# Optimization experiments

Measured on AMD Instinct MI355X. Metric: run time of the kernel, lower is better.

Reference implementation:

```python
import jax, jax.numpy as jnp
import numpy as np

B, N, H, D, HS, RS = 4, 512, 16, 64, 1024, 64  # HS = H*D, HSIZE_INSIDE == HSIZE
SCALE = 1.0 / float(np.sqrt(D))


def setup_inputs() -> dict:
    key = jax.random.key(0)
    ks = jax.random.split(key, 11)
    s = 0.02
    return {
        "v": jax.random.normal(ks[0], (B, N, HS), jnp.float32),
        "k": jax.random.normal(ks[1], (B, N, HS), jnp.float32),
        "q": jax.random.normal(ks[2], (B, N, HS), jnp.float32),
        "mask": jax.random.randint(ks[3], (B, 1, N, N), 0, 2).astype(bool),
        "rel_embed": jax.random.uniform(ks[4], (B, N, N, RS), jnp.float32),
        # weights stored as [in, out] (torch Linear applies x @ W.T)
        "Wv": jax.random.normal(ks[5], (HS, HS), jnp.float32) * s,
        "Wk": jax.random.normal(ks[6], (HS, HS), jnp.float32) * s,
        "Wq": jax.random.normal(ks[7], (HS, HS), jnp.float32) * s,
        "Wr": jax.random.normal(ks[8], (RS, H), jnp.float32) * s,
        "br": jax.random.normal(ks[9], (H,), jnp.float32) * s,
        "Wm": jax.random.normal(ks[10], (HS, HS), jnp.float32) * s,
    }


def reference(v, k, q, mask, rel_embed, Wv, Wk, Wq, Wr, br, Wm):
    b, nq, _ = q.shape

    def proj(x, W):  # [b, n, HS] -> [b, H, n, D]
        return (x @ W).reshape(b, -1, H, D).transpose(0, 2, 1, 3)

    vh, kh, qh = proj(v, Wv), proj(k, Wk), proj(q, Wq)
    # learned relative-position bias: relu -> clamp -> log, [b, H, nq, nk]
    r = jax.nn.relu(rel_embed @ Wr + br)
    bias = jnp.log(jnp.clip(r, 1e-6, None)).transpose(0, 3, 1, 2)
    scores = jnp.einsum('bhqd,bhkd->bhqk', qh, kh) * SCALE + bias
    scores = jnp.where(mask, jnp.float32(-1e9), scores)
    att = jax.nn.softmax(scores, axis=-1)  # dropout_r = 0
    atted = jnp.einsum('bhqk,bhkd->bhqd', att, vh)
    atted = atted.transpose(0, 2, 1, 3).reshape(b, nq, H * D)
    return atted @ Wm
```

## Files before the change

### kernel.cpp

```cpp
#include <hip/hip_runtime.h>
#include <hip/hip_bf16.h>


typedef __bf16 bf16_t;
typedef __bf16 bf16x8 __attribute__((ext_vector_type(8)));
typedef float f32x4 __attribute__((ext_vector_type(4)));

__device__ __forceinline__ f32x4 mfma16(bf16x8 a, bf16x8 b, f32x4 c) {
  return __builtin_amdgcn_mfma_f32_16x16x32_bf16(a, b, c, 0, 0, 0);
}
__device__ __forceinline__ f32x4 zero4() {
  f32x4 z; z[0] = 0.f; z[1] = 0.f; z[2] = 0.f; z[3] = 0.f; return z;
}

#define GLOAD_LDS16(gptr, lptr)                                                   \
  __builtin_amdgcn_global_load_lds(                                               \
      (const __attribute__((address_space(1))) unsigned int*)(gptr),              \
      (__attribute__((address_space(3))) unsigned int*)(lptr), 16, 0, 0)

__global__ __launch_bounds__(256) void prep_kernel(
    const float* __restrict__ W0, const float* __restrict__ W1,
    const float* __restrict__ W2, const float* __restrict__ W3,
    bf16_t* __restrict__ OutBase,
    const float* __restrict__ q, const float* __restrict__ k, const float* __restrict__ v,
    bf16_t* __restrict__ Qc, bf16_t* __restrict__ Kc, bf16_t* __restrict__ Vc,
    const unsigned int* __restrict__ mw, int* __restrict__ flag) {
  const int tid = threadIdx.x;
  if (blockIdx.x >= 1024) {
    const size_t gid = (size_t)(blockIdx.x - 1024) * 256 + tid;
    const int which = (int)(gid >> 18);
    const size_t off = (gid & 262143) * 8;
    const float* src = which == 0 ? q : which == 1 ? k : v;
    bf16_t* dst = which == 0 ? Qc : which == 1 ? Kc : Vc;
    const float scl = which == 0 ? 0.125f : 1.0f;
    float4 f0 = *(const float4*)(src + off);
    float4 f1 = *(const float4*)(src + off + 4);
    bf16x8 o;
    o[0] = (bf16_t)(f0.x * scl); o[1] = (bf16_t)(f0.y * scl);
    o[2] = (bf16_t)(f0.z * scl); o[3] = (bf16_t)(f0.w * scl);
    o[4] = (bf16_t)(f1.x * scl); o[5] = (bf16_t)(f1.y * scl);
    o[6] = (bf16_t)(f1.z * scl); o[7] = (bf16_t)(f1.w * scl);
    *(bf16x8*)(dst + off) = o;
    return;
  }
  const int wz = blockIdx.x >> 8, wy = (blockIdx.x >> 4) & 15, wx = blockIdx.x & 15;
  const float* W = wz == 0 ? W0 : wz == 1 ? W1 : wz == 2 ? W2 : W3;
  bf16_t* Ot = OutBase + (size_t)wz * 1024 * 1024;
  __shared__ float tile[64][68];
  __shared__ int sflag;
  const bool probe = (blockIdx.x == 0);
  if (probe && tid == 0) sflag = 0;
  const int i0 = wy * 64, j0 = wx * 64;
  const int ri = tid >> 2, rc = (tid & 3) * 16;
  const float* src = W + (size_t)(i0 + ri) * 1024 + j0 + rc;
#pragma unroll
  for (int qq = 0; qq < 4; ++qq) {
    float4 f = *(const float4*)(src + qq * 4);
    *(float4*)(&tile[ri][rc + qq * 4]) = f;
  }
  if (probe) {
    int any = 0;
    for (int i = tid; i < 4096; i += 256) any |= (mw[i] > 1u) ? 1 : 0;
    if (any) atomicOr(&sflag, 1);
  }
  __syncthreads();
  const int wj = tid >> 2, wc = (tid & 3) * 16;
  bf16x8 o0, o1;
#pragma unroll
  for (int s = 0; s < 8; ++s) o0[s] = (bf16_t)tile[wc + s][wj];
#pragma unroll
  for (int s = 0; s < 8; ++s) o1[s] = (bf16_t)tile[wc + 8 + s][wj];
  bf16_t* dst = Ot + (size_t)(j0 + wj) * 1024 + i0 + wc;
  *(bf16x8*)dst = o0;
  *(bf16x8*)(dst + 8) = o1;
  if (probe && tid == 0) *flag = sflag;
}

__global__ __launch_bounds__(256) void fat_kernel(
    const float* __restrict__ rel, const float* __restrict__ Wr,
    const float* __restrict__ br, const void* __restrict__ mask,
    const int* __restrict__ mflag, bf16_t* __restrict__ biasM,
    const bf16_t* __restrict__ Aq, const bf16_t* __restrict__ Ak, const bf16_t* __restrict__ Av,
    const bf16_t* __restrict__ Bq, const bf16_t* __restrict__ Bk, const bf16_t* __restrict__ Bv,
    bf16_t* __restrict__ Oq, bf16_t* __restrict__ Ok, bf16_t* __restrict__ Ov) {
  __shared__ __align__(16) bf16_t Asm[128 * 64];
  __shared__ __align__(16) bf16_t Bsm[128 * 64];
  const int tid = threadIdx.x, wid = tid >> 6, lane = tid & 63;
  const int lg = lane >> 4, lc = lane & 15;

  if (blockIdx.x < 2048) {
    const int pair = blockIdx.x;
    const int b = pair >> 9, qrow = pair & 511;
    const int isU8 = *mflag;
    bf16x8 wf[2];
#pragma unroll
    for (int kk = 0; kk < 2; ++kk)
#pragma unroll
      for (int j = 0; j < 8; ++j)
        wf[kk][j] = (bf16_t)Wr[(kk * 32 + lg * 8 + j) * 16 + lc];
    float brv[4];
#pragma unroll
    for (int j = 0; j < 4; ++j) brv[j] = br[lg * 4 + j];
    const float* relrow = rel + (size_t)pair * 512 * 64;
    const size_t mbase = (size_t)b * 512 * 512 + (size_t)qrow * 512;
    bf16_t* outb = biasM + (size_t)b * 16 * 512 * 512 + (size_t)qrow * 512;
#pragma unroll 4
    for (int kt = wid * 8; kt < wid * 8 + 8; ++kt) {
      const int k0 = kt * 16;
      const float* rrow = relrow + (size_t)(k0 + lc) * 64;
      f32x4 acc;
      acc[0] = brv[0]; acc[1] = brv[1]; acc[2] = brv[2]; acc[3] = brv[3];
#pragma unroll
      for (int kk = 0; kk < 2; ++kk) {
        const float4* s = (const float4*)(rrow + kk * 32 + lg * 8);
        float4 f0 = s[0], f1 = s[1];
        bf16x8 bfr;
        bfr[0] = (bf16_t)f0.x; bfr[1] = (bf16_t)f0.y; bfr[2] = (bf16_t)f0.z; bfr[3] = (bf16_t)f0.w;
        bfr[4] = (bf16_t)f1.x; bfr[5] = (bf16_t)f1.y; bfr[6] = (bf16_t)f1.z; bfr[7] = (bf16_t)f1.w;
        acc = mfma16(wf[kk], bfr, acc);
      }
      bool mb;
      if (isU8) mb = ((const unsigned char*)mask)[mbase + k0 + lc] != 0;
      else      mb = ((const int*)mask)[mbase + k0 + lc] != 0;
#pragma unroll
      for (int j = 0; j < 4; ++j) {
        const float valf = mb ? -1e9f : __logf(fmaxf(acc[j], 1e-6f));
        outb[(size_t)(lg * 4 + j) * 512 * 512 + k0 + lc] = (bf16_t)valf;
      }
    }
    return;
  }

  const int idx = blockIdx.x - 2048;
  const int z = idx >> 7, rem = idx & 127;
  const int byy = rem >> 3, bxx = rem & 7;
  const bf16_t* A = (z == 0) ? Aq : (z == 1) ? Ak : Av;
  const bf16_t* Bt = (z == 0) ? Bq : (z == 1) ? Bk : Bv;
  bf16_t* Out = (z == 0) ? Oq : (z == 1) ? Ok : Ov;
  const int m0 = byy * 128, n0 = bxx * 128;
  const int wm = (wid >> 1) * 64, wn = (wid & 1) * 64;
  const int sr = lane >> 3;
  const int scch = lane & 7;
  const int srcch = scch ^ sr;
  const bf16_t* Ap[4];
  const bf16_t* Bp[4];
#pragma unroll
  for (int i = 0; i < 4; ++i) {
    const int r = wid * 32 + i * 8 + sr;
    Ap[i] = A + (size_t)(m0 + r) * 1024 + srcch * 8;
    Bp[i] = Bt + (size_t)(n0 + r) * 1024 + srcch * 8;
  }
  f32x4 acc[4][4];
#pragma unroll
  for (int i = 0; i < 4; ++i)
#pragma unroll
    for (int j = 0; j < 4; ++j) acc[i][j] = zero4();

  for (int k0 = 0; k0 < 1024; k0 += 64) {
#pragma unroll
    for (int i = 0; i < 4; ++i) {
      GLOAD_LDS16(Ap[i] + k0, Asm + (wid * 32 + i * 8) * 64);
      GLOAD_LDS16(Bp[i] + k0, Bsm + (wid * 32 + i * 8) * 64);
    }
    __syncthreads();
#pragma unroll
    for (int kk = 0; kk < 2; ++kk) {
      bf16x8 af[4], bfv[4];
#pragma unroll
      for (int i = 0; i < 4; ++i) {
        const int ar = wm + i * 16 + lc;
        af[i] = *(const bf16x8*)(Asm + ar * 64 + ((kk * 4 + lg) ^ (ar & 7)) * 8);
        const int brr = wn + i * 16 + lc;
        bfv[i] = *(const bf16x8*)(Bsm + brr * 64 + ((kk * 4 + lg) ^ (brr & 7)) * 8);
      }
#pragma unroll
      for (int mi = 0; mi < 4; ++mi)
#pragma unroll
        for (int ni = 0; ni < 4; ++ni) acc[mi][ni] = mfma16(af[mi], bfv[ni], acc[mi][ni]);
    }
    __syncthreads();
  }
#pragma unroll
  for (int mi = 0; mi < 4; ++mi)
#pragma unroll
    for (int ni = 0; ni < 4; ++ni)
#pragma unroll
      for (int j = 0; j < 4; ++j) {
        const int m = m0 + wm + mi * 16 + lg * 4 + j;
        const int col = n0 + wn + ni * 16 + lc;
        const int b = m >> 9, n = m & 511;
        const int h = col >> 6, d = col & 63;
        Out[(((size_t)(b * 16 + h)) * 512 + n) * 64 + d] = (bf16_t)acc[mi][ni][j];
      }
}

__global__ __launch_bounds__(256) void attn_kernel(
    const bf16_t* __restrict__ Qh, const bf16_t* __restrict__ Kh,
    const bf16_t* __restrict__ Vh, const bf16_t* __restrict__ biasM,
    bf16_t* __restrict__ atted) {
  __shared__ __align__(16) bf16_t Ksm[2][64 * 64];
  __shared__ __align__(16) bf16_t Vtsm[2][64 * 88];
  __shared__ __align__(16) bf16_t Psm[4 * 16 * 64];
  const int tid = threadIdx.x, wid = tid >> 6, lane = tid & 63;
  const int lg = lane >> 4, lc = lane & 15;
  const int bid = blockIdx.x;
  const int qt = bid & 7, h = (bid >> 3) & 15, b = bid >> 7;
  const size_t headoff = (size_t)(b * 16 + h) * 512 * 64;
  const bf16_t* Qb = Qh + headoff;
  const bf16_t* Kb = Kh + headoff;
  const bf16_t* Vb = Vh + headoff;
  const int q0 = qt * 64 + wid * 16;
  const bf16_t* biasb = biasM + ((size_t)(b * 16 + h) * 512 + q0) * 512;

  bf16x8 qf[2];
#pragma unroll
  for (int kk = 0; kk < 2; ++kk)
    qf[kk] = *(const bf16x8*)(Qb + (size_t)(q0 + lc) * 64 + kk * 32 + lg * 8);

  f32x4 Oacc[4];
#pragma unroll
  for (int ds = 0; ds < 4; ++ds) Oacc[ds] = zero4();
  float mrun[4], lrun[4];
#pragma unroll
  for (int j = 0; j < 4; ++j) { mrun[j] = -INFINITY; lrun[j] = 0.f; }

  const int krow = tid & 63, kc0 = (tid >> 6) * 2;
  const int vn = tid & 63, vd0 = (tid >> 6) * 16;
  bf16_t* Pw = Psm + wid * 16 * 64;

#define STAGE(T, BUF)                                                          \
  do {                                                                         \
    const int kb_ = (T) * 64;                                                  \
    _Pragma("unroll") for (int ci = 0; ci < 2; ++ci) {                         \
      const int c_ = kc0 + ci;                                                 \
      bf16x8 kv_ = *(const bf16x8*)(Kb + (size_t)(kb_ + krow) * 64 + c_ * 8);  \
      *(bf16x8*)(Ksm[BUF] + krow * 64 + (c_ ^ (krow & 7)) * 8) = kv_;          \
    }                                                                          \
    bf16x8 v0_ = *(const bf16x8*)(Vb + (size_t)(kb_ + vn) * 64 + vd0);         \
    bf16x8 v1_ = *(const bf16x8*)(Vb + (size_t)(kb_ + vn) * 64 + vd0 + 8);     \
    _Pragma("unroll") for (int i = 0; i < 8; ++i)                              \
        Vtsm[BUF][(vd0 + i) * 88 + vn] = v0_[i];                               \
    _Pragma("unroll") for (int i = 0; i < 8; ++i)                              \
        Vtsm[BUF][(vd0 + 8 + i) * 88 + vn] = v1_[i];                           \
  } while (0)

  STAGE(0, 0);
  __syncthreads();

  for (int t = 0; t < 8; ++t) {
    const int cur = t & 1;
    if (t < 7) STAGE(t + 1, cur ^ 1);

    f32x4 sacc[4];
#pragma unroll
    for (int quad = 0; quad < 4; ++quad)
#pragma unroll
      for (int j = 0; j < 4; ++j)
        sacc[quad][j] = (float)biasb[(size_t)(lg * 4 + j) * 512 + t * 64 + quad * 16 + lc];

    const bf16_t* Kc = Ksm[cur];
#pragma unroll
    for (int quad = 0; quad < 4; ++quad) {
      const int kr = quad * 16 + lc;
#pragma unroll
      for (int kk = 0; kk < 2; ++kk) {
        bf16x8 kf = *(const bf16x8*)(Kc + kr * 64 + ((kk * 4 + lg) ^ (kr & 7)) * 8);
        sacc[quad] = mfma16(qf[kk], kf, sacc[quad]);
      }
    }

    float p[4][4];
#pragma unroll
    for (int j = 0; j < 4; ++j) {
      float tmax = fmaxf(fmaxf(sacc[0][j], sacc[1][j]), fmaxf(sacc[2][j], sacc[3][j]));
#pragma unroll
      for (int mm = 1; mm < 16; mm <<= 1) tmax = fmaxf(tmax, __shfl_xor(tmax, mm));
      const float mnew = fmaxf(mrun[j], tmax);
      const float sf = __expf(mrun[j] - mnew);
      mrun[j] = mnew;
      lrun[j] *= sf;
#pragma unroll
      for (int ds = 0; ds < 4; ++ds) Oacc[ds][j] *= sf;
      float psum = 0.f;
#pragma unroll
      for (int quad = 0; quad < 4; ++quad) {
        const float pv = __expf(sacc[quad][j] - mnew);
        p[quad][j] = pv;
        psum += pv;
      }
      lrun[j] += psum;
    }

#pragma unroll
    for (int quad = 0; quad < 4; ++quad)
#pragma unroll
      for (int j = 0; j < 4; ++j) {
        const int row = lg * 4 + j, col = quad * 16 + lc;
        Pw[row * 64 + ((col >> 3) ^ (row & 7)) * 8 + (col & 7)] = (bf16_t)p[quad][j];
      }

    const bf16_t* Vc = Vtsm[cur];
#pragma unroll
    for (int kk = 0; kk < 2; ++kk) {
      bf16x8 pf = *(const bf16x8*)(Pw + lc * 64 + ((kk * 4 + lg) ^ (lc & 7)) * 8);
#pragma unroll
      for (int ds = 0; ds < 4; ++ds) {
        bf16x8 vf = *(const bf16x8*)(Vc + (ds * 16 + lc) * 88 + kk * 32 + lg * 8);
        Oacc[ds] = mfma16(pf, vf, Oacc[ds]);
      }
    }
    __syncthreads();
  }
#undef STAGE

#pragma unroll
  for (int j = 0; j < 4; ++j) {
    float l = lrun[j];
#pragma unroll
    for (int mm = 1; mm < 16; mm <<= 1) l += __shfl_xor(l, mm);
    lrun[j] = 1.0f / l;
  }
#pragma unroll
  for (int ds = 0; ds < 4; ++ds)
#pragma unroll
    for (int j = 0; j < 4; ++j) {
      const int n = q0 + lg * 4 + j;
      const int d = ds * 16 + lc;
      atted[((size_t)b * 512 + n) * 1024 + h * 64 + d] = (bf16_t)(Oacc[ds][j] * lrun[j]);
    }
}

__global__ __launch_bounds__(256) void out_gemm2(
    const bf16_t* __restrict__ A, const bf16_t* __restrict__ Bt, float* __restrict__ Out) {
  __shared__ __align__(16) bf16_t Asm[128 * 64];
  __shared__ __align__(16) bf16_t Bsm[128 * 64];
  const int tid = threadIdx.x, wid = tid >> 6, lane = tid & 63;
  const int lg = lane >> 4, lc = lane & 15;
  const int m0 = blockIdx.y * 128, n0 = blockIdx.x * 128;
  const int wm = (wid >> 1) * 64, wn = (wid & 1) * 64;
  const int sr = lane >> 3, scch = lane & 7;
  const int srcch = scch ^ sr;
  const bf16_t* Ap[4];
  const bf16_t* Bp[4];
#pragma unroll
  for (int i = 0; i < 4; ++i) {
    const int r = wid * 32 + i * 8 + sr;
    Ap[i] = A + (size_t)(m0 + r) * 1024 + srcch * 8;
    Bp[i] = Bt + (size_t)(n0 + r) * 1024 + srcch * 8;
  }
  f32x4 acc[4][4];
#pragma unroll
  for (int i = 0; i < 4; ++i)
#pragma unroll
    for (int j = 0; j < 4; ++j) acc[i][j] = zero4();

  for (int k0 = 0; k0 < 1024; k0 += 64) {
#pragma unroll
    for (int i = 0; i < 4; ++i) {
      GLOAD_LDS16(Ap[i] + k0, Asm + (wid * 32 + i * 8) * 64);
      GLOAD_LDS16(Bp[i] + k0, Bsm + (wid * 32 + i * 8) * 64);
    }
    __syncthreads();
#pragma unroll
    for (int kk = 0; kk < 2; ++kk) {
      bf16x8 af[4], bfv[4];
#pragma unroll
      for (int i = 0; i < 4; ++i) {
        const int ar = wm + i * 16 + lc;
        af[i] = *(const bf16x8*)(Asm + ar * 64 + ((kk * 4 + lg) ^ (ar & 7)) * 8);
        const int brr = wn + i * 16 + lc;
        bfv[i] = *(const bf16x8*)(Bsm + brr * 64 + ((kk * 4 + lg) ^ (brr & 7)) * 8);
      }
#pragma unroll
      for (int mi = 0; mi < 4; ++mi)
#pragma unroll
        for (int ni = 0; ni < 4; ++ni) acc[mi][ni] = mfma16(af[mi], bfv[ni], acc[mi][ni]);
    }
    __syncthreads();
  }
#pragma unroll
  for (int mi = 0; mi < 4; ++mi)
#pragma unroll
    for (int ni = 0; ni < 4; ++ni)
#pragma unroll
      for (int j = 0; j < 4; ++j) {
        const int m = m0 + wm + mi * 16 + lg * 4 + j;
        const int col = n0 + wn + ni * 16 + lc;
        Out[(size_t)m * 1024 + col] = acc[mi][ni][j];
      }
}

extern "C" void kernel_launch(void* const* d_in, const int* in_sizes, int n_in,
                              void* d_out, int out_size, void* d_ws, size_t ws_size,
                              hipStream_t stream) {
  const float* v = (const float*)d_in[0];
  const float* k = (const float*)d_in[1];
  const float* q = (const float*)d_in[2];
  const void* mask = d_in[3];
  const float* rel = (const float*)d_in[4];
  const float* Wv = (const float*)d_in[5];
  const float* Wk = (const float*)d_in[6];
  const float* Wq = (const float*)d_in[7];
  const float* Wr = (const float*)d_in[8];
  const float* br = (const float*)d_in[9];
  const float* Wm = (const float*)d_in[10];

  char* ws = (char*)d_ws;
  bf16_t* Wt = (bf16_t*)ws;
  bf16_t* Qh = (bf16_t*)(ws + ((size_t)8 << 20));
  bf16_t* Kh = (bf16_t*)(ws + ((size_t)12 << 20));
  bf16_t* Vh = (bf16_t*)(ws + ((size_t)16 << 20));
  bf16_t* biasM = (bf16_t*)(ws + ((size_t)20 << 20));
  bf16_t* atted = (bf16_t*)(ws + ((size_t)52 << 20));
  bf16_t* Qc = (bf16_t*)(ws + ((size_t)56 << 20));
  bf16_t* Kc = (bf16_t*)(ws + ((size_t)60 << 20));
  bf16_t* Vc = (bf16_t*)(ws + ((size_t)64 << 20));
  int* mflag = (int*)(ws + ((size_t)68 << 20));
  bf16_t* Wvt = Wt + 0 * 1048576;
  bf16_t* Wkt = Wt + 1 * 1048576;
  bf16_t* Wqt = Wt + 2 * 1048576;
  bf16_t* Wmt = Wt + 3 * 1048576;

  prep_kernel<<<dim3(4096), 256, 0, stream>>>(Wv, Wk, Wq, Wm, Wt, q, k, v, Qc, Kc, Vc,
                                              (const unsigned int*)mask, mflag);
  fat_kernel<<<dim3(2432), 256, 0, stream>>>(rel, Wr, br, mask, mflag, biasM,
                                             Qc, Kc, Vc, Wqt, Wkt, Wvt, Qh, Kh, Vh);
  attn_kernel<<<dim3(512), 256, 0, stream>>>(Qh, Kh, Vh, biasM, atted);
  out_gemm2<<<dim3(8, 16), 256, 0, stream>>>(atted, Wmt, (float*)d_out);
}
```

Baseline: 144.8 us.

## Split bias kernel, stage bias output in LDS, and shrink GEMM tiles

Separates the fused bias/projection kernel into a dedicated bias kernel and a standalone projection GEMM. The bias kernel now stages results in shared memory and writes 16-byte vectors in a [b,q,h,k] layout, and the attention kernel's bias indexing is updated to match. This replaces scattered 2-byte stores strided across heads. The projection and output GEMMs drop from 128x128 to 64x64 tiles, giving more blocks to fill the CUs at the cost of less data reuse per block and an extra kernel launch.

```diff
diff --git a/kernel.cpp b/kernel.cpp
--- a/kernel.cpp
+++ b/kernel.cpp
@@ -76,114 +76,131 @@
   if (probe && tid == 0) *flag = sflag;
 }
 
-__global__ __launch_bounds__(256) void fat_kernel(
+__global__ __launch_bounds__(256) void bias_v4(
     const float* __restrict__ rel, const float* __restrict__ Wr,
     const float* __restrict__ br, const void* __restrict__ mask,
-    const int* __restrict__ mflag, bf16_t* __restrict__ biasM,
+    const int* __restrict__ mflag, bf16_t* __restrict__ biasM) {
+  __shared__ __align__(16) bf16_t outS[4][16 * 132];
+  const int tid = threadIdx.x, wid = tid >> 6, lane = tid & 63;
+  const int lg = lane >> 4, lc = lane & 15;
+  const int pair = blockIdx.x;
+  const int b = pair >> 9;
+  const int isU8 = *mflag;
+
+  bf16x8 wf[2];
+#pragma unroll
+  for (int kk = 0; kk < 2; ++kk)
+#pragma unroll
+    for (int j = 0; j < 8; ++j)
+      wf[kk][j] = (bf16_t)Wr[(kk * 32 + lg * 8 + j) * 16 + lc];
+  float brv[4];
+#pragma unroll
+  for (int j = 0; j < 4; ++j) brv[j] = br[lg * 4 + j];
+
+  const int kbase = wid * 128;
+  const float* relw = rel + (size_t)pair * 32768 + (size_t)kbase * 64;
+  const size_t mbase = (size_t)b * 262144 + (size_t)(pair & 511) * 512 + kbase;
+
+  unsigned mbits = 0;
+#pragma unroll
+  for (int it = 0; it < 8; ++it) {
+    const size_t mi = mbase + it * 16 + lc;
+    const bool mb = isU8 ? (((const unsigned char*)mask)[mi] != 0)
+                         : (((const int*)mask)[mi] != 0);
+    mbits |= (mb ? 1u : 0u) << it;
+  }
+
+  bf16_t* oS = outS[wid];
+#pragma unroll 2
+  for (int it = 0; it < 8; ++it) {
+    const float* rr = relw + (size_t)(it * 16 + lc) * 64 + lg * 8;
+    float4 f0 = *(const float4*)(rr);
+    float4 f1 = *(const float4*)(rr + 4);
+    float4 f2 = *(const float4*)(rr + 32);
+    float4 f3 = *(const float4*)(rr + 36);
+    bf16x8 bfr0, bfr1;
+    bfr0[0] = (bf16_t)f0.x; bfr0[1] = (bf16_t)f0.y; bfr0[2] = (bf16_t)f0.z; bfr0[3] = (bf16_t)f0.w;
+    bfr0[4] = (bf16_t)f1.x; bfr0[5] = (bf16_t)f1.y; bfr0[6] = (bf16_t)f1.z; bfr0[7] = (bf16_t)f1.w;
+    bfr1[0] = (bf16_t)f2.x; bfr1[1] = (bf16_t)f2.y; bfr1[2] = (bf16_t)f2.z; bfr1[3] = (bf16_t)f2.w;
+    bfr1[4] = (bf16_t)f3.x; bfr1[5] = (bf16_t)f3.y; bfr1[6] = (bf16_t)f3.z; bfr1[7] = (bf16_t)f3.w;
+    f32x4 acc;
+    acc[0] = brv[0]; acc[1] = brv[1]; acc[2] = brv[2]; acc[3] = brv[3];
+    acc = mfma16(wf[0], bfr0, acc);
+    acc = mfma16(wf[1], bfr1, acc);
+    const bool mb = (mbits >> it) & 1;
+#pragma unroll
+    for (int j = 0; j < 4; ++j) {
+      const float valf = mb ? -1e9f : __logf(fmaxf(acc[j], 1e-6f));
+      oS[(lg * 4 + j) * 132 + it * 16 + lc] = (bf16_t)valf;
+    }
+  }
+  const int h_ = lane >> 2, k8_ = lane & 3;
+  bf16_t* outb = biasM + (size_t)pair * 8192 + kbase;
+#pragma unroll
+  for (int u = 0; u < 4; ++u) {
+    bf16x8 ov = *(const bf16x8*)(oS + h_ * 132 + u * 32 + k8_ * 8);
+    *(bf16x8*)(outb + (size_t)h_ * 512 + u * 32 + k8_ * 8) = ov;
+  }
+}
+
+__global__ __launch_bounds__(256) void proj_gemm3(
     const bf16_t* __restrict__ Aq, const bf16_t* __restrict__ Ak, const bf16_t* __restrict__ Av,
     const bf16_t* __restrict__ Bq, const bf16_t* __restrict__ Bk, const bf16_t* __restrict__ Bv,
     bf16_t* __restrict__ Oq, bf16_t* __restrict__ Ok, bf16_t* __restrict__ Ov) {
-  __shared__ __align__(16) bf16_t Asm[128 * 64];
-  __shared__ __align__(16) bf16_t Bsm[128 * 64];
-  const int tid = threadIdx.x, wid = tid >> 6, lane = tid & 63;
-  const int lg = lane >> 4, lc = lane & 15;
-
-  if (blockIdx.x < 2048) {
-    const int pair = blockIdx.x;
-    const int b = pair >> 9, qrow = pair & 511;
-    const int isU8 = *mflag;
-    bf16x8 wf[2];
-#pragma unroll
-    for (int kk = 0; kk < 2; ++kk)
-#pragma unroll
-      for (int j = 0; j < 8; ++j)
-        wf[kk][j] = (bf16_t)Wr[(kk * 32 + lg * 8 + j) * 16 + lc];
-    float brv[4];
-#pragma unroll
-    for (int j = 0; j < 4; ++j) brv[j] = br[lg * 4 + j];
-    const float* relrow = rel + (size_t)pair * 512 * 64;
-    const size_t mbase = (size_t)b * 512 * 512 + (size_t)qrow * 512;
-    bf16_t* outb = biasM + (size_t)b * 16 * 512 * 512 + (size_t)qrow * 512;
-#pragma unroll 4
-    for (int kt = wid * 8; kt < wid * 8 + 8; ++kt) {
-      const int k0 = kt * 16;
-      const float* rrow = relrow + (size_t)(k0 + lc) * 64;
-      f32x4 acc;
-      acc[0] = brv[0]; acc[1] = brv[1]; acc[2] = brv[2]; acc[3] = brv[3];
-#pragma unroll
-      for (int kk = 0; kk < 2; ++kk) {
-        const float4* s = (const float4*)(rrow + kk * 32 + lg * 8);
-        float4 f0 = s[0], f1 = s[1];
-        bf16x8 bfr;
-        bfr[0] = (bf16_t)f0.x; bfr[1] = (bf16_t)f0.y; bfr[2] = (bf16_t)f0.z; bfr[3] = (bf16_t)f0.w;
-        bfr[4] = (bf16_t)f1.x; bfr[5] = (bf16_t)f1.y; bfr[6] = (bf16_t)f1.z; bfr[7] = (bf16_t)f1.w;
-        acc = mfma16(wf[kk], bfr, acc);
-      }
-      bool mb;
-      if (isU8) mb = ((const unsigned char*)mask)[mbase + k0 + lc] != 0;
-      else      mb = ((const int*)mask)[mbase + k0 + lc] != 0;
-#pragma unroll
-      for (int j = 0; j < 4; ++j) {
-        const float valf = mb ? -1e9f : __logf(fmaxf(acc[j], 1e-6f));
-        outb[(size_t)(lg * 4 + j) * 512 * 512 + k0 + lc] = (bf16_t)valf;
-      }
-    }
-    return;
-  }
-
-  const int idx = blockIdx.x - 2048;
-  const int z = idx >> 7, rem = idx & 127;
-  const int byy = rem >> 3, bxx = rem & 7;
+  const int z = blockIdx.z;
   const bf16_t* A = (z == 0) ? Aq : (z == 1) ? Ak : Av;
   const bf16_t* Bt = (z == 0) ? Bq : (z == 1) ? Bk : Bv;
   bf16_t* Out = (z == 0) ? Oq : (z == 1) ? Ok : Ov;
-  const int m0 = byy * 128, n0 = bxx * 128;
-  const int wm = (wid >> 1) * 64, wn = (wid & 1) * 64;
-  const int sr = lane >> 3;
-  const int scch = lane & 7;
+  __shared__ __align__(16) bf16_t Asm[64 * 64];
+  __shared__ __align__(16) bf16_t Bsm[64 * 64];
+  const int tid = threadIdx.x, wid = tid >> 6, lane = tid & 63;
+  const int lg = lane >> 4, lc = lane & 15;
+  const int m0 = blockIdx.y * 64, n0 = blockIdx.x * 64;
+  const int wm = (wid >> 1) * 32, wn = (wid & 1) * 32;
+  const int sr = lane >> 3, scch = lane & 7;
   const int srcch = scch ^ sr;
-  const bf16_t* Ap[4];
-  const bf16_t* Bp[4];
-#pragma unroll
-  for (int i = 0; i < 4; ++i) {
-    const int r = wid * 32 + i * 8 + sr;
+  const bf16_t* Ap[2];
+  const bf16_t* Bp[2];
+#pragma unroll
+  for (int i = 0; i < 2; ++i) {
+    const int r = wid * 16 + i * 8 + sr;
     Ap[i] = A + (size_t)(m0 + r) * 1024 + srcch * 8;
     Bp[i] = Bt + (size_t)(n0 + r) * 1024 + srcch * 8;
   }
-  f32x4 acc[4][4];
-#pragma unroll
-  for (int i = 0; i < 4; ++i)
-#pragma unroll
-    for (int j = 0; j < 4; ++j) acc[i][j] = zero4();
+  f32x4 acc[2][2];
+#pragma unroll
+  for (int i = 0; i < 2; ++i)
+#pragma unroll
+    for (int j = 0; j < 2; ++j) acc[i][j] = zero4();
 
   for (int k0 = 0; k0 < 1024; k0 += 64) {
 #pragma unroll
-    for (int i = 0; i < 4; ++i) {
-      GLOAD_LDS16(Ap[i] + k0, Asm + (wid * 32 + i * 8) * 64);
-      GLOAD_LDS16(Bp[i] + k0, Bsm + (wid * 32 + i * 8) * 64);
+    for (int i = 0; i < 2; ++i) {
+      GLOAD_LDS16(Ap[i] + k0, Asm + (wid * 16 + i * 8) * 64);
+      GLOAD_LDS16(Bp[i] + k0, Bsm + (wid * 16 + i * 8) * 64);
     }
     __syncthreads();
 #pragma unroll
     for (int kk = 0; kk < 2; ++kk) {
-      bf16x8 af[4], bfv[4];
-#pragma unroll
-      for (int i = 0; i < 4; ++i) {
+      bf16x8 af[2], bfv[2];
+#pragma unroll
+      for (int i = 0; i < 2; ++i) {
         const int ar = wm + i * 16 + lc;
         af[i] = *(const bf16x8*)(Asm + ar * 64 + ((kk * 4 + lg) ^ (ar & 7)) * 8);
         const int brr = wn + i * 16 + lc;
         bfv[i] = *(const bf16x8*)(Bsm + brr * 64 + ((kk * 4 + lg) ^ (brr & 7)) * 8);
       }
 #pragma unroll
-      for (int mi = 0; mi < 4; ++mi)
-#pragma unroll
-        for (int ni = 0; ni < 4; ++ni) acc[mi][ni] = mfma16(af[mi], bfv[ni], acc[mi][ni]);
+      for (int mi = 0; mi < 2; ++mi)
+#pragma unroll
+        for (int ni = 0; ni < 2; ++ni) acc[mi][ni] = mfma16(af[mi], bfv[ni], acc[mi][ni]);
     }
     __syncthreads();
   }
 #pragma unroll
-  for (int mi = 0; mi < 4; ++mi)
-#pragma unroll
-    for (int ni = 0; ni < 4; ++ni)
+  for (int mi = 0; mi < 2; ++mi)
+#pragma unroll
+    for (int ni = 0; ni < 2; ++ni)
 #pragma unroll
       for (int j = 0; j < 4; ++j) {
         const int m = m0 + wm + mi * 16 + lg * 4 + j;
@@ -210,7 +227,7 @@
   const bf16_t* Kb = Kh + headoff;
   const bf16_t* Vb = Vh + headoff;
   const int q0 = qt * 64 + wid * 16;
-  const bf16_t* biasb = biasM + ((size_t)(b * 16 + h) * 512 + q0) * 512;
+  const bf16_t* biasb = biasM + (((size_t)(b * 512 + q0)) * 16 + h) * 512;
 
   bf16x8 qf[2];
 #pragma unroll
@@ -256,7 +273,8 @@
     for (int quad = 0; quad < 4; ++quad)
 #pragma unroll
       for (int j = 0; j < 4; ++j)
-        sacc[quad][j] = (float)biasb[(size_t)(lg * 4 + j) * 512 + t * 64 + quad * 16 + lc];
+        sacc[quad][j] =
+            (float)biasb[(size_t)(lg * 4 + j) * 8192 + t * 64 + quad * 16 + lc];
 
     const bf16_t* Kc = Ksm[cur];
 #pragma unroll
@@ -330,58 +348,58 @@
     }
 }
 
-__global__ __launch_bounds__(256) void out_gemm2(
+__global__ __launch_bounds__(256) void out_gemm3(
     const bf16_t* __restrict__ A, const bf16_t* __restrict__ Bt, float* __restrict__ Out) {
-  __shared__ __align__(16) bf16_t Asm[128 * 64];
-  __shared__ __align__(16) bf16_t Bsm[128 * 64];
+  __shared__ __align__(16) bf16_t Asm[64 * 64];
+  __shared__ __align__(16) bf16_t Bsm[64 * 64];
   const int tid = threadIdx.x, wid = tid >> 6, lane = tid & 63;
   const int lg = lane >> 4, lc = lane & 15;
-  const int m0 = blockIdx.y * 128, n0 = blockIdx.x * 128;
-  const int wm = (wid >> 1) * 64, wn = (wid & 1) * 64;
+  const int m0 = blockIdx.y * 64, n0 = blockIdx.x * 64;
+  const int wm = (wid >> 1) * 32, wn = (wid & 1) * 32;
   const int sr = lane >> 3, scch = lane & 7;
   const int srcch = scch ^ sr;
-  const bf16_t* Ap[4];
-  const bf16_t* Bp[4];
-#pragma unroll
-  for (int i = 0; i < 4; ++i) {
-    const int r = wid * 32 + i * 8 + sr;
+  const bf16_t* Ap[2];
+  const bf16_t* Bp[2];
+#pragma unroll
+  for (int i = 0; i < 2; ++i) {
+    const int r = wid * 16 + i * 8 + sr;
     Ap[i] = A + (size_t)(m0 + r) * 1024 + srcch * 8;
     Bp[i] = Bt + (size_t)(n0 + r) * 1024 + srcch * 8;
   }
-  f32x4 acc[4][4];
-#pragma unroll
-  for (int i = 0; i < 4; ++i)
-#pragma unroll
-    for (int j = 0; j < 4; ++j) acc[i][j] = zero4();
+  f32x4 acc[2][2];
+#pragma unroll
+  for (int i = 0; i < 2; ++i)
+#pragma unroll
+    for (int j = 0; j < 2; ++j) acc[i][j] = zero4();
 
   for (int k0 = 0; k0 < 1024; k0 += 64) {
 #pragma unroll
-    for (int i = 0; i < 4; ++i) {
-      GLOAD_LDS16(Ap[i] + k0, Asm + (wid * 32 + i * 8) * 64);
-      GLOAD_LDS16(Bp[i] + k0, Bsm + (wid * 32 + i * 8) * 64);
+    for (int i = 0; i < 2; ++i) {
+      GLOAD_LDS16(Ap[i] + k0, Asm + (wid * 16 + i * 8) * 64);
+      GLOAD_LDS16(Bp[i] + k0, Bsm + (wid * 16 + i * 8) * 64);
     }
     __syncthreads();
 #pragma unroll
     for (int kk = 0; kk < 2; ++kk) {
-      bf16x8 af[4], bfv[4];
-#pragma unroll
-      for (int i = 0; i < 4; ++i) {
+      bf16x8 af[2], bfv[2];
+#pragma unroll
+      for (int i = 0; i < 2; ++i) {
         const int ar = wm + i * 16 + lc;
         af[i] = *(const bf16x8*)(Asm + ar * 64 + ((kk * 4 + lg) ^ (ar & 7)) * 8);
         const int brr = wn + i * 16 + lc;
         bfv[i] = *(const bf16x8*)(Bsm + brr * 64 + ((kk * 4 + lg) ^ (brr & 7)) * 8);
       }
 #pragma unroll
-      for (int mi = 0; mi < 4; ++mi)
-#pragma unroll
-        for (int ni = 0; ni < 4; ++ni) acc[mi][ni] = mfma16(af[mi], bfv[ni], acc[mi][ni]);
+      for (int mi = 0; mi < 2; ++mi)
+#pragma unroll
+        for (int ni = 0; ni < 2; ++ni) acc[mi][ni] = mfma16(af[mi], bfv[ni], acc[mi][ni]);
     }
     __syncthreads();
   }
 #pragma unroll
-  for (int mi = 0; mi < 4; ++mi)
-#pragma unroll
-    for (int ni = 0; ni < 4; ++ni)
+  for (int mi = 0; mi < 2; ++mi)
+#pragma unroll
+    for (int ni = 0; ni < 2; ++ni)
 #pragma unroll
       for (int j = 0; j < 4; ++j) {
         const int m = m0 + wm + mi * 16 + lg * 4 + j;
@@ -423,8 +441,8 @@
 
   prep_kernel<<<dim3(4096), 256, 0, stream>>>(Wv, Wk, Wq, Wm, Wt, q, k, v, Qc, Kc, Vc,
                                               (const unsigned int*)mask, mflag);
-  fat_kernel<<<dim3(2432), 256, 0, stream>>>(rel, Wr, br, mask, mflag, biasM,
-                                             Qc, Kc, Vc, Wqt, Wkt, Wvt, Qh, Kh, Vh);
+  bias_v4<<<dim3(2048), 256, 0, stream>>>(rel, Wr, br, mask, mflag, biasM);
+  proj_gemm3<<<dim3(16, 32, 3), 256, 0, stream>>>(Qc, Kc, Vc, Wqt, Wkt, Wvt, Qh, Kh, Vh);
   attn_kernel<<<dim3(512), 256, 0, stream>>>(Qh, Kh, Vh, biasM, atted);
-  out_gemm2<<<dim3(8, 16), 256, 0, stream>>>(atted, Wmt, (float*)d_out);
-}
+  out_gemm3<<<dim3(16, 32), 256, 0, stream>>>(atted, Wmt, (float*)d_out);
+}
```

Measured after the change: 145.9 us. Within noise of the previous version (+0.8%).
